# Optimization experiments

Hardware: AMD Instinct MI355X
Metric: run time of the kernel (lower is better)

The kernel has to match this reference:

```python
import jax, jax.numpy as jnp
import numpy as np

D_MODEL = 1024

def setup_inputs() -> dict:
    key = jax.random.key(0)
    ks = jax.random.split(key, 8)
    B, S, D = 8, 2048, D_MODEL
    scale = 1.0 / np.sqrt(D)
    return {
        "x1": jax.random.normal(ks[0], (B, S, D), dtype=jnp.float32),
        "x2": jax.random.normal(ks[1], (B, S, D), dtype=jnp.float32),
        "Wq": jax.random.normal(ks[2], (D, D), dtype=jnp.float32) * scale,
        "bq": jnp.zeros((D,), dtype=jnp.float32),
        "Wk": jax.random.normal(ks[3], (D, D), dtype=jnp.float32) * scale,
        "bk": jnp.zeros((D,), dtype=jnp.float32),
        "Wv": jax.random.normal(ks[4], (D, D), dtype=jnp.float32) * scale,
        "bv": jnp.zeros((D,), dtype=jnp.float32),
    }

def reference(x1, x2, Wq, bq, Wk, bk, Wv, bv):
    # q1: [B, Sq, D]; k2, v2: [B, Sk, D]
    q1 = jnp.einsum('bsd,de->bse', x1, Wq) + bq
    k2 = jnp.einsum('bsd,de->bse', x2, Wk) + bk
    v2 = jnp.einsum('bsd,de->bse', x2, Wv) + bv
    scale = 1.0 / np.sqrt(q1.shape[-1]).astype(np.float32)
    scores = jnp.einsum('bqd,bkd->bqk', q1, k2) * scale  # [B, Sq, Sk]
    probs = jax.nn.softmax(scores, axis=-1)
    return jnp.einsum('bqk,bkd->bqd', probs, v2)
```

## Files before the change

kernel.cpp:

```cpp
#include <hip/hip_runtime.h>
#include <hip/hip_bf16.h>
#include <hip/hip_fp16.h>

typedef __attribute__((ext_vector_type(8))) short short8;
typedef __attribute__((ext_vector_type(4))) float f32x4;

#define DEVI __device__ __forceinline__

DEVI unsigned short f2bf(float f){
  __hip_bfloat16 h = __float2bfloat16(f);
  unsigned short u; __builtin_memcpy(&u, &h, 2); return u;
}

__global__ void cast_f32_bf16(const float* __restrict__ in, unsigned short* __restrict__ out, int n4){
  int stride = gridDim.x * blockDim.x;
  for (int i = blockIdx.x*blockDim.x + threadIdx.x; i < n4; i += stride){
    float4 f = reinterpret_cast<const float4*>(in)[i];
    ushort4 o;
    o.x = f2bf(f.x); o.y = f2bf(f.y); o.z = f2bf(f.z); o.w = f2bf(f.w);
    reinterpret_cast<ushort4*>(out)[i] = o;
  }
}

__global__ void transpose_cast_w(const float* __restrict__ W, unsigned short* __restrict__ WT, int K, int N){
  __shared__ float tile[32][33];
  int bn = blockIdx.x*32, bk = blockIdx.y*32;
  int tx = threadIdx.x & 31, ty = threadIdx.x >> 5;
  for (int r=0;r<32;r+=8)
    tile[ty+r][tx] = W[(long)(bk+ty+r)*N + bn+tx];
  __syncthreads();
  for (int r=0;r<32;r+=8)
    WT[(long)(bn+ty+r)*K + bk+tx] = (short)f2bf(tile[tx][ty+r]);
}

DEVI void stage16(const short* gsrc, short* lbase){
  __builtin_amdgcn_global_load_lds(
      (const __attribute__((address_space(1))) unsigned int*)gsrc,
      (__attribute__((address_space(3))) unsigned int*)lbase, 16, 0, 0);
}

DEVI void stage_half(const short* __restrict__ gtile, int ldK, int koff,
                     short* lds_block, int w, int lane){
  const int r  = lane >> 2;
  const int kk = ((lane & 3) * 8) ^ ((lane >= 32) ? 16 : 0);
  #pragma unroll
  for (int i = 0; i < 2; ++i){
    const int c = i*8 + w;
    const short* src = gtile + (long)(c*16 + r) * ldK + koff + kk;
    stage16(src, lds_block + c*512);
  }
}

DEVI short8 ldsRd(const short* lds, int blk, int rowblk, int lane){
  const int la = lane & 15;
  int q = rowblk*1024 + la*64 + ((lane>>4)<<4);
  q ^= (la >= 8) ? 32 : 0;
  return *reinterpret_cast<const short8*>(lds + blk*8192 + (q>>1));
}

template<int OT, int BIAS>
__global__ __launch_bounds__(512, 2)
void gemm8(const short* __restrict__ A, const short* __restrict__ Bt,
           const float* __restrict__ bias, void* __restrict__ Cv,
           int N, int K, long sA, long sB, long sC, float scale, int nx, int ny)
{
  extern __shared__ short lds[];
  const int nwg = gridDim.x;
  const int cpx = nwg >> 3;
  const int wg  = (blockIdx.x & 7)*cpx + (blockIdx.x >> 3);
  const int bx  = wg % nx;
  const int tmp = wg / nx;
  const int by  = tmp % ny;
  const long bz = tmp / ny;
  A  += bz * sA;
  Bt += bz * sB;
  const int m0 = bx * 256, n0 = by * 256;
  const short* Ab = A  + (long)m0 * K;
  const short* Bb = Bt + (long)n0 * K;

  const int t = threadIdx.x, lane = t & 63, w = t >> 6;
  const int wr = w >> 2, wc = w & 3;

  f32x4 acc[8][4] = {};
  short8 bv[4];

  const int NT = K >> 6;
  const int niter = NT >> 1;

  stage_half(Ab, K, 0,  lds + 0,     w, lane);
  stage_half(Bb, K, 0,  lds + 16384, w, lane);
  stage_half(Ab, K, 32, lds + 8192,  w, lane);
  stage_half(Bb, K, 32, lds + 24576, w, lane);
  stage_half(Ab, K, 64, lds + 32768, w, lane);
  stage_half(Bb, K, 64, lds + 49152, w, lane);
  asm volatile("s_waitcnt vmcnt(4)" ::: "memory");
  __builtin_amdgcn_s_barrier();

#define PH(CBUF, QM, QK, SPTR, SKOFF, SBLK, TAILVM) do {                        \
    short8 a0_ = ldsRd(lds, (CBUF)*4 + (QK), wr*8 + (QM)*4 + 0, lane);          \
    short8 a1_ = ldsRd(lds, (CBUF)*4 + (QK), wr*8 + (QM)*4 + 1, lane);          \
    short8 a2_ = ldsRd(lds, (CBUF)*4 + (QK), wr*8 + (QM)*4 + 2, lane);          \
    short8 a3_ = ldsRd(lds, (CBUF)*4 + (QK), wr*8 + (QM)*4 + 3, lane);          \
    if ((QM) == 0){                                                             \
      bv[0] = ldsRd(lds, (CBUF)*4 + 2 + (QK), wc*4 + 0, lane);                  \
      bv[1] = ldsRd(lds, (CBUF)*4 + 2 + (QK), wc*4 + 1, lane);                  \
      bv[2] = ldsRd(lds, (CBUF)*4 + 2 + (QK), wc*4 + 2, lane);                  \
      bv[3] = ldsRd(lds, (CBUF)*4 + 2 + (QK), wc*4 + 3, lane);                  \
    }                                                                           \
    stage_half(SPTR, K, (SKOFF), lds + (SBLK), w, lane);                        \
    __builtin_amdgcn_s_barrier();                                               \
    asm volatile("s_waitcnt lgkmcnt(0)" ::: "memory");                          \
    __builtin_amdgcn_s_setprio(1);                                              \
    { short8 av_[4] = {a0_, a1_, a2_, a3_};                                     \
      _Pragma("unroll")                                                         \
      for (int i_=0;i_<4;i_++){                                                 \
        _Pragma("unroll")                                                       \
        for (int j_=0;j_<4;j_++)                                                \
          acc[(QM)*4+i_][j_] = __builtin_amdgcn_mfma_f32_16x16x32_bf16(         \
              av_[i_], bv[j_], acc[(QM)*4+i_][j_], 0, 0, 0);                    \
      }                                                                         \
    }                                                                           \
    __builtin_amdgcn_s_setprio(0);                                              \
    if (TAILVM) asm volatile("s_waitcnt vmcnt(4)" ::: "memory");                \
    __builtin_amdgcn_s_barrier();                                               \
  } while(0)

  for (int it = 0; it < niter; ++it){
    const int u  = it*2;
    const int k1 = ((u+1) % NT)*64;
    const int k2 = ((u+2) % NT)*64;
    const int k3 = ((u+3) % NT)*64;
    PH(0, 0, 0, Ab, k1+32, 40960, 0);
    PH(0, 1, 0, Bb, k1+32, 57344, 0);
    PH(0, 0, 1, Ab, k2,    0,     0);
    PH(0, 1, 1, Bb, k2,    16384, 1);
    PH(1, 0, 0, Ab, k2+32, 8192,  0);
    PH(1, 1, 0, Bb, k2+32, 24576, 0);
    PH(1, 0, 1, Ab, k3,    32768, 0);
    PH(1, 1, 1, Bb, k3,    49152, 1);
  }
#undef PH

  const int rowb = m0 + wr*128 + ((lane>>4)<<2);
  const int colb = n0 + wc*64 + (lane & 15);
  #pragma unroll
  for (int mi=0; mi<8; ++mi){
    #pragma unroll
    for (int nj=0; nj<4; ++nj){
      const int col = colb + nj*16;
      float badd = (BIAS==1) ? bias[col] : 0.0f;
      #pragma unroll
      for (int j=0;j<4;j++){
        const int row = rowb + mi*16 + j;
        float v = acc[mi][nj][j] * scale + badd;
        if (BIAS==2) v += bias[row];
        const long idx = bz*sC + (long)row*N + col;
        if constexpr (OT==0) ((float*)Cv)[idx] = v;
        else if constexpr (OT==1) ((__half*)Cv)[idx] = __float2half(v);
        else ((unsigned short*)Cv)[idx] = f2bf(v);
      }
    }
  }
}

__global__ void softmax_rows(unsigned short* __restrict__ SP, int cols){
  const long row = blockIdx.x;
  unsigned short* rp = SP + row * cols;
  const int t = threadIdx.x, lane = t & 63, w = t >> 6;
  short8 raw = *reinterpret_cast<const short8*>(rp + t*8);
  float v[8];
  #pragma unroll
  for (int i=0;i<8;i++){
    unsigned short us = (unsigned short)raw[i];
    __half h; __builtin_memcpy(&h, &us, 2);
    v[i] = __half2float(h);
  }
  float m = v[0];
  #pragma unroll
  for (int i=1;i<8;i++) m = fmaxf(m, v[i]);
  #pragma unroll
  for (int o=32;o;o>>=1) m = fmaxf(m, __shfl_down(m, o));
  __shared__ float red[8];
  if (lane==0) red[w] = m;
  __syncthreads();
  if (t==0) red[4] = fmaxf(fmaxf(red[0],red[1]), fmaxf(red[2],red[3]));
  __syncthreads();
  const float rowmax = red[4];
  float s = 0.f;
  #pragma unroll
  for (int i=0;i<8;i++){ v[i] = __expf(v[i]-rowmax); s += v[i]; }
  #pragma unroll
  for (int o=32;o;o>>=1) s += __shfl_down(s, o);
  if (lane==0) red[w] = s;
  __syncthreads();
  if (t==0) red[5] = red[0]+red[1]+red[2]+red[3];
  __syncthreads();
  const float inv = 1.0f / red[5];
  short8 outp;
  #pragma unroll
  for (int i=0;i<8;i++) outp[i] = (short)f2bf(v[i]*inv);
  *reinterpret_cast<short8*>(rp + t*8) = outp;
}

extern "C" void kernel_launch(void* const* d_in, const int* in_sizes, int n_in,
                              void* d_out, int out_size, void* d_ws, size_t ws_size,
                              hipStream_t stream)
{
  const int B = 8, S = 2048, D = 1024;
  const int BS = B * S;
  const float* x1 = (const float*)d_in[0];
  const float* x2 = (const float*)d_in[1];
  const float* Wq = (const float*)d_in[2];
  const float* bq = (const float*)d_in[3];
  const float* Wk = (const float*)d_in[4];
  const float* bk = (const float*)d_in[5];
  const float* Wv = (const float*)d_in[6];
  const float* bv = (const float*)d_in[7];

  char* ws = (char*)d_ws;
  const size_t MB = 1024*1024;
  short*          x1b = (short*)(ws);
  short*          x2b = (short*)(ws + 32*MB);
  unsigned short* Sc  = (unsigned short*)ws;
  short*          q   = (short*)(ws + 64*MB);
  short*          k   = (short*)(ws + 96*MB);
  short*          vT  = (short*)(ws + 128*MB);
  short*          WqT = (short*)(ws + 160*MB);
  short*          WkT = (short*)(ws + 162*MB);
  short*          WvT = (short*)(ws + 164*MB);

  const size_t SH = 131072;

  cast_f32_bf16<<<4096,256,0,stream>>>(x1, (unsigned short*)x1b, BS*D/4);
  cast_f32_bf16<<<4096,256,0,stream>>>(x2, (unsigned short*)x2b, BS*D/4);
  transpose_cast_w<<<dim3(32,32),256,0,stream>>>(Wq, (unsigned short*)WqT, D, D);
  transpose_cast_w<<<dim3(32,32),256,0,stream>>>(Wk, (unsigned short*)WkT, D, D);
  transpose_cast_w<<<dim3(32,32),256,0,stream>>>(Wv, (unsigned short*)WvT, D, D);

  gemm8<2,1><<<256, 512, SH, stream>>>(x2b, WkT, bk, k, D, D, 0,0,0, 1.0f, 64, 4);
  gemm8<2,2><<<256, 512, SH, stream>>>(WvT, x2b, bv, vT, S, D, 0, (long)S*D, (long)D*S, 1.0f, 4, 8);
  gemm8<2,1><<<256, 512, SH, stream>>>(x1b, WqT, bq, q, D, D, 0,0,0, 1.0f, 64, 4);
  gemm8<1,0><<<512, 512, SH, stream>>>(q, k, nullptr, Sc, S, D,
                                       (long)S*D, (long)S*D, (long)S*S, 0.03125f, 8, 8);
  softmax_rows<<<BS,256,0,stream>>>(Sc, S);
  gemm8<0,0><<<256, 512, SH, stream>>>((short*)Sc, vT, nullptr, d_out, D, S,
                                       (long)S*S, (long)D*S, (long)S*D, 1.0f, 8, 4);
}
```

Before: 332.0 us.

## Stage GEMM epilogue through LDS for coalesced vector stores and precompute addresses

```diff
diff --git a/kernel.cpp b/kernel.cpp
--- a/kernel.cpp
+++ b/kernel.cpp
@@ -39,23 +39,9 @@
       (__attribute__((address_space(3))) unsigned int*)lbase, 16, 0, 0);
 }
 
-DEVI void stage_half(const short* __restrict__ gtile, int ldK, int koff,
-                     short* lds_block, int w, int lane){
-  const int r  = lane >> 2;
-  const int kk = ((lane & 3) * 8) ^ ((lane >= 32) ? 16 : 0);
-  #pragma unroll
-  for (int i = 0; i < 2; ++i){
-    const int c = i*8 + w;
-    const short* src = gtile + (long)(c*16 + r) * ldK + koff + kk;
-    stage16(src, lds_block + c*512);
-  }
-}
-
-DEVI short8 ldsRd(const short* lds, int blk, int rowblk, int lane){
-  const int la = lane & 15;
-  int q = rowblk*1024 + la*64 + ((lane>>4)<<4);
-  q ^= (la >= 8) ? 32 : 0;
-  return *reinterpret_cast<const short8*>(lds + blk*8192 + (q>>1));
+DEVI void stage2(const short* base, long o0, long o1, short* blk, int w){
+  stage16(base + o0, blk + w*512);
+  stage16(base + o1, blk + (8+w)*512);
 }
 
 template<int OT, int BIAS>
@@ -72,43 +58,53 @@
   const int tmp = wg / nx;
   const int by  = tmp % ny;
   const long bz = tmp / ny;
-  A  += bz * sA;
-  Bt += bz * sB;
   const int m0 = bx * 256, n0 = by * 256;
-  const short* Ab = A  + (long)m0 * K;
-  const short* Bb = Bt + (long)n0 * K;
+  const short* Ab = A  + bz*sA + (long)m0 * K;
+  const short* Bb = Bt + bz*sB + (long)n0 * K;
 
   const int t = threadIdx.x, lane = t & 63, w = t >> 6;
   const int wr = w >> 2, wc = w & 3;
 
+  const int rr = lane >> 2;
+  const int kk = ((lane & 3) * 8) ^ ((lane & 32) ? 16 : 0);
+  const long off0 = (long)(( w     )*16 + rr) * K + kk;
+  const long off1 = (long)(( 8 + w )*16 + rr) * K + kk;
+
+  const int la = lane & 15;
+  const int lsw = (la*64 + ((lane>>4)<<4)) ^ ((la>=8)?32:0);
+  const short* AP = lds + (lsw>>1) + wr*4096;
+  const short* BP = lds + (lsw>>1) + 16384 + wc*2048;
+
   f32x4 acc[8][4] = {};
   short8 bv[4];
 
   const int NT = K >> 6;
   const int niter = NT >> 1;
 
-  stage_half(Ab, K, 0,  lds + 0,     w, lane);
-  stage_half(Bb, K, 0,  lds + 16384, w, lane);
-  stage_half(Ab, K, 32, lds + 8192,  w, lane);
-  stage_half(Bb, K, 32, lds + 24576, w, lane);
-  stage_half(Ab, K, 64, lds + 32768, w, lane);
-  stage_half(Bb, K, 64, lds + 49152, w, lane);
+  stage2(Ab,      off0, off1, lds + 0,     w);
+  stage2(Bb,      off0, off1, lds + 16384, w);
+  stage2(Ab + 32, off0, off1, lds + 8192,  w);
+  stage2(Bb + 32, off0, off1, lds + 24576, w);
+  stage2(Ab + 64, off0, off1, lds + 32768, w);
+  stage2(Bb + 64, off0, off1, lds + 49152, w);
   asm volatile("s_waitcnt vmcnt(4)" ::: "memory");
-  __builtin_amdgcn_s_barrier();
-
-#define PH(CBUF, QM, QK, SPTR, SKOFF, SBLK, TAILVM) do {                        \
-    short8 a0_ = ldsRd(lds, (CBUF)*4 + (QK), wr*8 + (QM)*4 + 0, lane);          \
-    short8 a1_ = ldsRd(lds, (CBUF)*4 + (QK), wr*8 + (QM)*4 + 1, lane);          \
-    short8 a2_ = ldsRd(lds, (CBUF)*4 + (QK), wr*8 + (QM)*4 + 2, lane);          \
-    short8 a3_ = ldsRd(lds, (CBUF)*4 + (QK), wr*8 + (QM)*4 + 3, lane);          \
+  asm volatile("s_barrier" ::: "memory");
+
+#define PH(CBUF, QM, QK, SBASE, SOFF, SBLK, TAILVM) do {                        \
+    const short* ap_ = AP + (CBUF)*32768 + (QK)*8192 + (QM)*2048;               \
+    short8 a0_ = *reinterpret_cast<const short8*>(ap_ + 0*512);                 \
+    short8 a1_ = *reinterpret_cast<const short8*>(ap_ + 1*512);                 \
+    short8 a2_ = *reinterpret_cast<const short8*>(ap_ + 2*512);                 \
+    short8 a3_ = *reinterpret_cast<const short8*>(ap_ + 3*512);                 \
     if ((QM) == 0){                                                             \
-      bv[0] = ldsRd(lds, (CBUF)*4 + 2 + (QK), wc*4 + 0, lane);                  \
-      bv[1] = ldsRd(lds, (CBUF)*4 + 2 + (QK), wc*4 + 1, lane);                  \
-      bv[2] = ldsRd(lds, (CBUF)*4 + 2 + (QK), wc*4 + 2, lane);                  \
-      bv[3] = ldsRd(lds, (CBUF)*4 + 2 + (QK), wc*4 + 3, lane);                  \
+      const short* bp_ = BP + (CBUF)*32768 + (QK)*8192;                         \
+      bv[0] = *reinterpret_cast<const short8*>(bp_ + 0*512);                    \
+      bv[1] = *reinterpret_cast<const short8*>(bp_ + 1*512);                    \
+      bv[2] = *reinterpret_cast<const short8*>(bp_ + 2*512);                    \
+      bv[3] = *reinterpret_cast<const short8*>(bp_ + 3*512);                    \
     }                                                                           \
-    stage_half(SPTR, K, (SKOFF), lds + (SBLK), w, lane);                        \
-    __builtin_amdgcn_s_barrier();                                               \
+    stage2((SBASE) + (SOFF), off0, off1, lds + (SBLK), w);                      \
+    asm volatile("s_barrier" ::: "memory");                                     \
     asm volatile("s_waitcnt lgkmcnt(0)" ::: "memory");                          \
     __builtin_amdgcn_s_setprio(1);                                              \
     { short8 av_[4] = {a0_, a1_, a2_, a3_};                                     \
@@ -122,14 +118,15 @@
     }                                                                           \
     __builtin_amdgcn_s_setprio(0);                                              \
     if (TAILVM) asm volatile("s_waitcnt vmcnt(4)" ::: "memory");                \
-    __builtin_amdgcn_s_barrier();                                               \
+    asm volatile("s_barrier" ::: "memory");                                     \
   } while(0)
 
   for (int it = 0; it < niter; ++it){
     const int u  = it*2;
-    const int k1 = ((u+1) % NT)*64;
-    const int k2 = ((u+2) % NT)*64;
-    const int k3 = ((u+3) % NT)*64;
+    int u1 = u+1; if (u1 >= NT) u1 -= NT;
+    int u2 = u+2; if (u2 >= NT) u2 -= NT;
+    int u3 = u+3; if (u3 >= NT) u3 -= NT;
+    const int k1 = u1*64, k2 = u2*64, k3 = u3*64;
     PH(0, 0, 0, Ab, k1+32, 40960, 0);
     PH(0, 1, 0, Bb, k1+32, 57344, 0);
     PH(0, 0, 1, Ab, k2,    0,     0);
@@ -141,23 +138,51 @@
   }
 #undef PH
 
-  const int rowb = m0 + wr*128 + ((lane>>4)<<2);
-  const int colb = n0 + wc*64 + (lane & 15);
-  #pragma unroll
-  for (int mi=0; mi<8; ++mi){
+  {
+    char* sb = (char*)lds;
+    constexpr int STRB = (OT==0) ? 1056 : 544;
+    const int tr = t >> 4, tcE = (t & 15) * 16;
+    const int grow = m0 + (tr>>4)*128 + (tr&15);
     #pragma unroll
-    for (int nj=0; nj<4; ++nj){
-      const int col = colb + nj*16;
-      float badd = (BIAS==1) ? bias[col] : 0.0f;
+    for (int mi = 0; mi < 8; ++mi){
+      __syncthreads();
       #pragma unroll
-      for (int j=0;j<4;j++){
-        const int row = rowb + mi*16 + j;
-        float v = acc[mi][nj][j] * scale + badd;
-        if (BIAS==2) v += bias[row];
-        const long idx = bz*sC + (long)row*N + col;
-        if constexpr (OT==0) ((float*)Cv)[idx] = v;
-        else if constexpr (OT==1) ((__half*)Cv)[idx] = __float2half(v);
-        else ((unsigned short*)Cv)[idx] = f2bf(v);
+      for (int nj = 0; nj < 4; ++nj){
+        const int c = wc*64 + la + nj*16;
+        float badd = (BIAS==1) ? bias[n0 + c] : 0.0f;
+        #pragma unroll
+        for (int j = 0; j < 4; ++j){
+          const int lr = wr*16 + ((lane>>4)<<2) + j;
+          float v = acc[mi][nj][j] * scale + badd;
+          if (BIAS==2) v += bias[m0 + (lr>>4)*128 + mi*16 + (lr&15)];
+          if constexpr (OT==0){
+            const int byte = lr*STRB + ((((c>>2) ^ (lr&15)))<<4) + (c&3)*4;
+            *reinterpret_cast<float*>(sb + byte) = v;
+          } else if constexpr (OT==1){
+            const int byte = lr*STRB + ((((c>>3) ^ (lr&15)))<<4) + (c&7)*2;
+            *reinterpret_cast<__half*>(sb + byte) = __float2half(v);
+          } else {
+            const int byte = lr*STRB + ((((c>>3) ^ (lr&15)))<<4) + (c&7)*2;
+            *reinterpret_cast<unsigned short*>(sb + byte) = f2bf(v);
+          }
+        }
+      }
+      __syncthreads();
+      const long gbase = bz*sC + (long)(grow + mi*16)*N + n0 + tcE;
+      if constexpr (OT==0){
+        const int cb = tcE >> 2;
+        #pragma unroll
+        for (int i=0;i<4;i++){
+          f32x4 vv = *reinterpret_cast<const f32x4*>(sb + tr*STRB + (((cb+i)^(tr&15))<<4));
+          *reinterpret_cast<f32x4*>((float*)Cv + gbase + i*4) = vv;
+        }
+      } else {
+        const int cb = tcE >> 3;
+        #pragma unroll
+        for (int i=0;i<2;i++){
+          short8 vv = *reinterpret_cast<const short8*>(sb + tr*STRB + (((cb+i)^(tr&15))<<4));
+          *reinterpret_cast<short8*>((unsigned short*)Cv + gbase + i*8) = vv;
+        }
       }
     }
   }
```

New measurement: 346.5 us. 4.4% more time.
